# Performance work log

Hardware: AMD Instinct MI355X
Metric: run time of the kernel (lower is better)

## Reference

```python
import jax, jax.numpy as jnp
import numpy as np

B, L, D = 1, 4096, 2048
H, KV, HD = 16, 4, 128
WINDOW = 1024
ROPE_BASE = 10000.0


def _rms_norm(x, scale):
    var = jnp.mean(jnp.square(x), axis=-1, keepdims=True)
    return x * jax.lax.rsqrt(var + 1e-6) * scale


def _apply_rope(x, positions, base_frequency):
    # x: (B, L, N, HD); positions: (B, L)
    head_dim = x.shape[-1]
    half = head_dim // 2
    freq_exp = 2.0 * jnp.arange(half, dtype=jnp.float32) / head_dim
    timescale = base_frequency ** freq_exp                       # (half,)
    sinusoid = positions[..., None].astype(jnp.float32) / timescale  # (B, L, half)
    sin = jnp.sin(sinusoid)[:, :, None, :]                       # (B, L, 1, half)
    cos = jnp.cos(sinusoid)[:, :, None, :]
    x1, x2 = x[..., :half], x[..., half:]
    return jnp.concatenate([x1 * cos - x2 * sin, x2 * cos + x1 * sin], axis=-1)


def setup_inputs() -> dict:
    key = jax.random.key(0)
    ks = jax.random.split(key, 5)
    x = jax.random.normal(ks[0], (B, L, D), dtype=jnp.float32)
    positions = jnp.broadcast_to(jnp.arange(L, dtype=jnp.int32), (B, L))
    s = D ** -0.5
    Wq = jax.random.normal(ks[1], (D, H * HD), dtype=jnp.float32) * s
    Wk = jax.random.normal(ks[2], (D, KV * HD), dtype=jnp.float32) * s
    Wv = jax.random.normal(ks[3], (D, KV * HD), dtype=jnp.float32) * s
    Wo = jax.random.normal(ks[4], (H * HD, D), dtype=jnp.float32) * ((H * HD) ** -0.5)
    q_scale = jnp.ones((HD,), dtype=jnp.float32)
    k_scale = jnp.ones((HD,), dtype=jnp.float32)
    return {"x": x, "positions": positions, "Wq": Wq, "Wk": Wk, "Wv": Wv,
            "Wo": Wo, "q_scale": q_scale, "k_scale": k_scale}


def reference(x, positions, Wq, Wk, Wv, Wo, q_scale, k_scale):
    q = (x @ Wq).reshape(B, L, H, HD)
    k = (x @ Wk).reshape(B, L, KV, HD)
    v = (x @ Wv).reshape(B, L, KV, HD)

    q = _apply_rope(_rms_norm(q, q_scale), positions, ROPE_BASE)
    k = _apply_rope(_rms_norm(k, k_scale), positions, ROPE_BASE)

    rep = H // KV
    k = jnp.repeat(k, rep, axis=2)   # (B, L, H, HD)
    v = jnp.repeat(v, rep, axis=2)

    scale = HD ** -0.5
    scores = jnp.einsum('bqhd,bkhd->bhqk', q, k) * scale  # (B, H, L, L)

    idx = jnp.arange(L)
    causal = idx[:, None] >= idx[None, :]
    window = idx[None, :] >= idx[:, None] - (WINDOW - 1)
    mask = causal & window
    scores = jnp.where(mask[None, None, :, :], scores, jnp.finfo(scores.dtype).min)
    attn = jax.nn.softmax(scores, axis=-1)

    out = jnp.einsum('bhqk,bkhd->bqhd', attn, v).reshape(B, L, H * HD)
    return out @ Wo
```

## Files before the change

kernel.cpp:

```cpp
#include <hip/hip_runtime.h>
#include <cstdint>
#include <cstddef>

typedef unsigned short u16;
typedef __attribute__((ext_vector_type(4))) float  float4v;
typedef __attribute__((ext_vector_type(4))) int    int4v;
typedef __attribute__((ext_vector_type(8))) short  short8v;
typedef __attribute__((ext_vector_type(4))) short  short4v;

#define L_SEQ 4096
#define NH 16
#define NKV 4
#define WND 1024

static __device__ __forceinline__ u16 f2bf(float f) {
  union { float f; unsigned u; } v; v.f = f;
  unsigned r = (v.u + 0x7FFFu + ((v.u >> 16) & 1u)) >> 16;
  return (u16)r;
}
static __device__ __forceinline__ u16 f2bf_fast(float f) {
  union { float f; unsigned u; } v; v.f = f;
  return (u16)((v.u + 0x8000u) >> 16);
}
static __device__ __forceinline__ float bf2f(u16 b) {
  union { unsigned u; float f; } v; v.u = ((unsigned)b) << 16;
  return v.f;
}

__global__ __launch_bounds__(256) void k_cvt(const float* __restrict__ in,
                                             u16* __restrict__ out, int n4) {
  int i = blockIdx.x * 256 + threadIdx.x;
  if (i >= n4) return;
  float4v v = ((const float4v*)in)[i];
  short4v o;
  o[0] = (short)f2bf(v[0]); o[1] = (short)f2bf(v[1]);
  o[2] = (short)f2bf(v[2]); o[3] = (short)f2bf(v[3]);
  ((short4v*)out)[i] = o;
}

__global__ __launch_bounds__(256) void k_transpose64(const float* __restrict__ in,
                                                     u16* __restrict__ out,
                                                     int K, int N, int row_off) {
  __shared__ float tile[64][65];
  int n0 = blockIdx.x * 64, k0 = blockIdx.y * 64;
  int tx = threadIdx.x & 63, ty = threadIdx.x >> 6;
#pragma unroll
  for (int i = 0; i < 16; i++)
    tile[ty + i*4][tx] = in[(size_t)(k0 + ty + i*4)*N + n0 + tx];
  __syncthreads();
#pragma unroll
  for (int i = 0; i < 16; i++)
    out[(size_t)(row_off + n0 + ty + i*4)*K + k0 + tx] = f2bf(tile[tx][ty + i*4]);
}

__global__ __launch_bounds__(256) void k_vtrans(const u16* __restrict__ qkvb,
                                                u16* __restrict__ vT) {
  __shared__ u16 tile[64][66];
  int p0 = blockIdx.x * 64, d0 = blockIdx.y * 64;
  int tx = threadIdx.x & 63, ty = threadIdx.x >> 6;
#pragma unroll
  for (int i = 0; i < 16; i++)
    tile[ty + i*4][tx] = qkvb[(size_t)(p0 + ty + i*4)*3072 + 2560 + d0 + tx];
  __syncthreads();
#pragma unroll
  for (int i = 0; i < 16; i++)
    vT[(size_t)(d0 + ty + i*4)*L_SEQ + p0 + tx] = tile[tx][ty + i*4];
}

template<int BF16_OUT>
__global__ __launch_bounds__(256) void k_gemm_bt(const u16* __restrict__ A,
                                                 const u16* __restrict__ B,
                                                 void* __restrict__ Cv,
                                                 int M, int N, int K) {
  __shared__ alignas(16) u16 As[128*64];
  __shared__ alignas(16) u16 Bs[128*64];
  int tid = threadIdx.x;
  int lane = tid & 63, wave = tid >> 6;
  int lr = lane & 15, lg = lane >> 4;
  int m0 = blockIdx.y * 128, n0 = blockIdx.x * 128;
  int wm = (wave >> 1) * 64, wn = (wave & 1) * 64;

  float4v acc[4][4];
#pragma unroll
  for (int i = 0; i < 4; i++)
#pragma unroll
    for (int j = 0; j < 4; j++)
#pragma unroll
      for (int r = 0; r < 4; r++) acc[i][j][r] = 0.f;

  for (int kt = 0; kt < K; kt += 64) {
    __syncthreads();
#pragma unroll
    for (int it = 0; it < 4; it++) {
      int s = it*256 + tid;
      int row = s >> 3, j = s & 7;
      int col = ((j ^ (row & 7)) << 3);
      __builtin_amdgcn_global_load_lds(
          (const __attribute__((address_space(1))) void*)(A + (size_t)(m0 + row)*K + kt + col),
          (__attribute__((address_space(3))) void*)(&As[s * 8]), 16, 0, 0);
      __builtin_amdgcn_global_load_lds(
          (const __attribute__((address_space(1))) void*)(B + (size_t)(n0 + row)*K + kt + col),
          (__attribute__((address_space(3))) void*)(&Bs[s * 8]), 16, 0, 0);
    }
    __syncthreads();
#pragma unroll
    for (int half = 0; half < 2; half++) {
      short8v af[4], bf[4];
#pragma unroll
      for (int i = 0; i < 4; i++) {
        int row = wm + i*16 + lr;
        af[i] = *(const short8v*)(&As[row*64 + ((((half<<2)|lg) ^ (row & 7)) << 3)]);
      }
#pragma unroll
      for (int j = 0; j < 4; j++) {
        int row = wn + j*16 + lr;
        bf[j] = *(const short8v*)(&Bs[row*64 + ((((half<<2)|lg) ^ (row & 7)) << 3)]);
      }
#pragma unroll
      for (int i = 0; i < 4; i++)
#pragma unroll
        for (int j = 0; j < 4; j++)
          acc[i][j] = __builtin_amdgcn_mfma_f32_16x16x32_bf16(af[i], bf[j], acc[i][j], 0, 0, 0);
    }
  }
#pragma unroll
  for (int i = 0; i < 4; i++)
#pragma unroll
    for (int j = 0; j < 4; j++)
#pragma unroll
      for (int r = 0; r < 4; r++) {
        size_t idx = (size_t)(m0 + wm + i*16 + lg*4 + r)*N + (n0 + wn + j*16 + lr);
        if (BF16_OUT) ((u16*)Cv)[idx] = f2bf(acc[i][j][r]);
        else          ((float*)Cv)[idx] = acc[i][j][r];
      }
}

__global__ __launch_bounds__(256) void k_qknorm(const u16* __restrict__ qkvb,
    const int* __restrict__ positions, const float* __restrict__ q_scale,
    const float* __restrict__ k_scale, u16* __restrict__ qb,
    u16* __restrict__ kb) {
  int p = blockIdx.x * 4 + (threadIdx.x >> 6);
  int l = threadIdx.x & 63;
  const float LOG2_BASE = 13.287712379549449f;
  float ang = (float)positions[p] * exp2f(-(float)l * (LOG2_BASE / 64.0f));
  float sn, cs; sincosf(ang, &sn, &cs);
  float qs1 = q_scale[l], qs2 = q_scale[l + 64];
  float ks1 = k_scale[l], ks2 = k_scale[l + 64];
  const u16* base = qkvb + (size_t)p * 3072;
  const float qsc = 0.12751741505539613f;
#pragma unroll
  for (int h = 0; h < 16; h++) {
    float x1 = bf2f(base[h*128 + l]), x2 = bf2f(base[h*128 + l + 64]);
    float ss = x1*x1 + x2*x2;
#pragma unroll
    for (int m = 1; m < 64; m <<= 1) ss += __shfl_xor(ss, m);
    float rinv = rsqrtf(ss * (1.0f/128.0f) + 1e-6f);
    x1 *= rinv * qs1; x2 *= rinv * qs2;
    u16* dst = qb + ((size_t)p*NH + h)*128;
    dst[l]      = f2bf((x1*cs - x2*sn) * qsc);
    dst[l + 64] = f2bf((x2*cs + x1*sn) * qsc);
  }
#pragma unroll
  for (int g = 0; g < 4; g++) {
    float x1 = bf2f(base[2048 + g*128 + l]), x2 = bf2f(base[2048 + g*128 + l + 64]);
    float ss = x1*x1 + x2*x2;
#pragma unroll
    for (int m = 1; m < 64; m <<= 1) ss += __shfl_xor(ss, m);
    float rinv = rsqrtf(ss * (1.0f/128.0f) + 1e-6f);
    x1 *= rinv * ks1; x2 *= rinv * ks2;
    u16* dst = kb + ((size_t)p*NKV + g)*128;
    dst[l]      = f2bf(x1*cs - x2*sn);
    dst[l + 64] = f2bf(x2*cs + x1*sn);
  }
}

__global__ __launch_bounds__(256) void k_attn(const u16* __restrict__ qb,
    const u16* __restrict__ kb, const u16* __restrict__ vT,
    u16* __restrict__ ob) {
  __shared__ alignas(16) u16 Ks[64*128];
  __shared__ alignas(16) u16 Vs[128*64];
  __shared__ alignas(16) u16 Pw[4][2][16*72];
  int tid = threadIdx.x;
  int lane = tid & 63, wave = tid >> 6;
  int lr = lane & 15, lg = lane >> 4;
  int flat = blockIdx.x;
  int xcd = flat & 7, slot = flat >> 3;
  int gh = xcd >> 1;
  int q0 = ((xcd & 1) * 64 + slot) * 32;
  int h = gh * 4 + wave;

  short8v qf[2][4];
#pragma unroll
  for (int m = 0; m < 2; m++) {
    const u16* qrow = qb + ((size_t)(q0 + m*16 + lr)*NH + h)*128 + lg*8;
#pragma unroll
    for (int t = 0; t < 4; t++) qf[m][t] = *(const short8v*)(qrow + t*32);
  }

  const short one_bf = (short)0x3F80;
  const short8v ones = {one_bf,one_bf,one_bf,one_bf,one_bf,one_bf,one_bf,one_bf};

  float4v O[9][2];
#pragma unroll
  for (int dt = 0; dt < 9; dt++)
#pragma unroll
    for (int m = 0; m < 2; m++)
#pragma unroll
      for (int r = 0; r < 4; r++) O[dt][m][r] = 0.f;

  int kstart = q0 - (WND - 1); if (kstart < 0) kstart = 0; kstart &= ~63;
  for (int kt = kstart; kt < q0 + 32; kt += 64) {
    __syncthreads();
#pragma unroll
    for (int it = 0; it < 4; it++) {
      int s = it*256 + tid;
      { int row = s >> 4, j = s & 15, col = (j ^ (row & 15)) << 3;
        __builtin_amdgcn_global_load_lds(
            (const __attribute__((address_space(1))) void*)(kb + (size_t)(kt + row)*512 + gh*128 + col),
            (__attribute__((address_space(3))) void*)(&Ks[s * 8]), 16, 0, 0); }
      { int row = s >> 3, j = s & 7, col = (j ^ (row & 7)) << 3;
        __builtin_amdgcn_global_load_lds(
            (const __attribute__((address_space(1))) void*)(vT + (size_t)(gh*128 + row)*L_SEQ + kt + col),
            (__attribute__((address_space(3))) void*)(&Vs[s * 8]), 16, 0, 0); }
    }
    __syncthreads();

    float4v S[2][4];
#pragma unroll
    for (int m = 0; m < 2; m++)
#pragma unroll
      for (int t2 = 0; t2 < 4; t2++)
#pragma unroll
        for (int r = 0; r < 4; r++) S[m][t2][r] = 0.f;
#pragma unroll
    for (int t2 = 0; t2 < 4; t2++) {
      int row = t2*16 + lr;
#pragma unroll
      for (int t = 0; t < 4; t++) {
        short8v kf = *(const short8v*)(&Ks[row*128 + (((t*4 + lg) ^ (row & 15)) << 3)]);
        S[0][t2] = __builtin_amdgcn_mfma_f32_16x16x32_bf16(qf[0][t], kf, S[0][t2], 0, 0, 0);
        S[1][t2] = __builtin_amdgcn_mfma_f32_16x16x32_bf16(qf[1][t], kf, S[1][t2], 0, 0, 0);
      }
    }

    bool need_mask = (kt + 64 > q0) || (kt < q0 - (WND - 32));
    if (need_mask) {
#pragma unroll
      for (int m = 0; m < 2; m++)
#pragma unroll
        for (int r = 0; r < 4; r++) {
          int pos = q0 + m*16 + lg*4 + r;
#pragma unroll
          for (int t2 = 0; t2 < 4; t2++) {
            int key = kt + t2*16 + lr;
            float p = (key > pos || key < pos - (WND - 1)) ? 0.f : exp2f(S[m][t2][r]);
            Pw[wave][m][(lg*4 + r)*72 + t2*16 + lr] = f2bf_fast(p);
          }
        }
    } else {
#pragma unroll
      for (int m = 0; m < 2; m++)
#pragma unroll
        for (int r = 0; r < 4; r++)
#pragma unroll
          for (int t2 = 0; t2 < 4; t2++)
            Pw[wave][m][(lg*4 + r)*72 + t2*16 + lr] = f2bf_fast(exp2f(S[m][t2][r]));
    }

    short8v pf[2][2];
#pragma unroll
    for (int m = 0; m < 2; m++)
#pragma unroll
      for (int sub = 0; sub < 2; sub++)
        pf[m][sub] = *(const short8v*)(&Pw[wave][m][lr*72 + sub*32 + lg*8]);

#pragma unroll
    for (int sub = 0; sub < 2; sub++)
#pragma unroll
      for (int dt = 0; dt < 8; dt++) {
        int row = dt*16 + lr;
        short8v vf = *(const short8v*)(&Vs[row*64 + (((sub*4 + lg) ^ (row & 7)) << 3)]);
        O[dt][0] = __builtin_amdgcn_mfma_f32_16x16x32_bf16(pf[0][sub], vf, O[dt][0], 0, 0, 0);
        O[dt][1] = __builtin_amdgcn_mfma_f32_16x16x32_bf16(pf[1][sub], vf, O[dt][1], 0, 0, 0);
      }
#pragma unroll
    for (int m = 0; m < 2; m++) {
      O[8][m] = __builtin_amdgcn_mfma_f32_16x16x32_bf16(pf[m][0], ones, O[8][m], 0, 0, 0);
      O[8][m] = __builtin_amdgcn_mfma_f32_16x16x32_bf16(pf[m][1], ones, O[8][m], 0, 0, 0);
    }
  }

#pragma unroll
  for (int m = 0; m < 2; m++)
#pragma unroll
    for (int r = 0; r < 4; r++) {
      float inv = 1.0f / O[8][m][r];
#pragma unroll
      for (int dt = 0; dt < 8; dt++)
        ob[((size_t)(q0 + m*16 + lg*4 + r)*NH + h)*128 + dt*16 + lr] =
            f2bf(O[dt][m][r] * inv);
    }
}

extern "C" void kernel_launch(void* const* d_in, const int* in_sizes, int n_in,
                              void* d_out, int out_size, void* d_ws, size_t ws_size,
                              hipStream_t stream) {
  (void)in_sizes; (void)n_in; (void)out_size; (void)ws_size;
  const float* x        = (const float*)d_in[0];
  const int*   positions= (const int*)d_in[1];
  const float* Wq       = (const float*)d_in[2];
  const float* Wk       = (const float*)d_in[3];
  const float* Wv       = (const float*)d_in[4];
  const float* Wo       = (const float*)d_in[5];
  const float* q_scale  = (const float*)d_in[6];
  const float* k_scale  = (const float*)d_in[7];
  float* out = (float*)d_out;

  char* ws = (char*)d_ws;
  u16* xb   = (u16*)ws; ws += (size_t)4096*2048*2;
  u16* Wt   = (u16*)ws; ws += (size_t)3072*2048*2;
  u16* Wot  = (u16*)ws; ws += (size_t)2048*2048*2;
  u16* qkvb = (u16*)ws; ws += (size_t)4096*3072*2;
  u16* qb   = (u16*)ws; ws += (size_t)4096*2048*2;
  u16* kb   = (u16*)ws; ws += (size_t)4096*512*2;
  u16* vT   = (u16*)ws; ws += (size_t)4096*512*2;
  u16* ob   = qkvb;

  k_cvt<<<8192, 256, 0, stream>>>(x, xb, 2097152);
  k_transpose64<<<dim3(32,32), 256, 0, stream>>>(Wq, Wt, 2048, 2048, 0);
  k_transpose64<<<dim3(8,32),  256, 0, stream>>>(Wk, Wt, 2048, 512, 2048);
  k_transpose64<<<dim3(8,32),  256, 0, stream>>>(Wv, Wt, 2048, 512, 2560);
  k_transpose64<<<dim3(32,32), 256, 0, stream>>>(Wo, Wot, 2048, 2048, 0);
  k_gemm_bt<1><<<dim3(24,32), 256, 0, stream>>>(xb, Wt, qkvb, 4096, 3072, 2048);
  k_qknorm<<<1024, 256, 0, stream>>>(qkvb, positions, q_scale, k_scale, qb, kb);
  k_vtrans<<<dim3(64,8), 256, 0, stream>>>(qkvb, vT);
  k_attn<<<512, 256, 0, stream>>>(qb, kb, vT, ob);
  k_gemm_bt<0><<<dim3(16,32), 256, 0, stream>>>(ob, Wot, out, 4096, 2048, 2048);
}
```

Measured before the change: 296.7 us.

## Replace GEMM with 256x256 double-buffered 8-wave pipelined kernel

Replaces the 128x128 single-buffered GEMM with a 256x256 tile kernel using 8 waves, double-buffered LDS, and staged global-to-LDS loads interleaved with MFMA phases. It also remaps workgroups into XCD-aware chunks and raises MFMA priority with setprio. The goal is to hide load latency behind compute and raise data reuse per tile. In exchange, the grid shrinks to 192 and 128 workgroups, which may underfill the 256 CUs, and LDS use rises to 128KB per block.

```diff
diff --git a/kernel.cpp b/kernel.cpp
--- a/kernel.cpp
+++ b/kernel.cpp
@@ -67,71 +67,169 @@
     vT[(size_t)(d0 + ty + i*4)*L_SEQ + p0 + tx] = tile[tx][ty + i*4];
 }
 
-template<int BF16_OUT>
-__global__ __launch_bounds__(256) void k_gemm_bt(const u16* __restrict__ A,
-                                                 const u16* __restrict__ B,
-                                                 void* __restrict__ Cv,
-                                                 int M, int N, int K) {
-  __shared__ alignas(16) u16 As[128*64];
-  __shared__ alignas(16) u16 Bs[128*64];
+template<int KDIM>
+static __device__ __forceinline__ void stage_half(const u16* __restrict__ g,
+                                                  u16* lds, int tid) {
+#pragma unroll
+  for (int it = 0; it < 2; ++it) {
+    int s = it * 512 + tid;
+    int row = s >> 3, slot = s & 7;
+    __builtin_amdgcn_global_load_lds(
+        (const __attribute__((address_space(1))) void*)(g + (size_t)row * KDIM + ((slot ^ (row & 7)) << 3)),
+        (__attribute__((address_space(3))) void*)(lds + s * 8), 16, 0, 0);
+  }
+}
+
+template<int BF16_OUT, int KDIM>
+__global__ __launch_bounds__(512, 2) void k_gemm8(const u16* __restrict__ A,
+                                                  const u16* __restrict__ B,
+                                                  void* __restrict__ Cv,
+                                                  int N) {
+  constexpr int NT = KDIM >> 6;
+  __shared__ alignas(16) u16 As[2][256 * 64];
+  __shared__ alignas(16) u16 Bs[2][256 * 64];
   int tid = threadIdx.x;
   int lane = tid & 63, wave = tid >> 6;
   int lr = lane & 15, lg = lane >> 4;
-  int m0 = blockIdx.y * 128, n0 = blockIdx.x * 128;
-  int wm = (wave >> 1) * 64, wn = (wave & 1) * 64;
-
-  float4v acc[4][4];
-#pragma unroll
-  for (int i = 0; i < 4; i++)
+  int wm = (wave >> 2) * 128, wn = (wave & 3) * 64;
+
+  int nwg = gridDim.x * gridDim.y;
+  int orig = blockIdx.y * gridDim.x + blockIdx.x;
+  int cpx = nwg >> 3;
+  int wg = (orig & 7) * cpx + (orig >> 3);
+  int tn = wg % gridDim.x, tm = wg / gridDim.x;
+  int m0 = tm * 256, n0 = tn * 256;
+
+  const u16* Ag = A + (size_t)m0 * KDIM;
+  const u16* Bg = B + (size_t)n0 * KDIM;
+
+  float4v acc[8][4];
+#pragma unroll
+  for (int i = 0; i < 8; i++)
 #pragma unroll
     for (int j = 0; j < 4; j++)
 #pragma unroll
       for (int r = 0; r < 4; r++) acc[i][j][r] = 0.f;
 
-  for (int kt = 0; kt < K; kt += 64) {
-    __syncthreads();
-#pragma unroll
-    for (int it = 0; it < 4; it++) {
-      int s = it*256 + tid;
-      int row = s >> 3, j = s & 7;
-      int col = ((j ^ (row & 7)) << 3);
-      __builtin_amdgcn_global_load_lds(
-          (const __attribute__((address_space(1))) void*)(A + (size_t)(m0 + row)*K + kt + col),
-          (__attribute__((address_space(3))) void*)(&As[s * 8]), 16, 0, 0);
-      __builtin_amdgcn_global_load_lds(
-          (const __attribute__((address_space(1))) void*)(B + (size_t)(n0 + row)*K + kt + col),
-          (__attribute__((address_space(3))) void*)(&Bs[s * 8]), 16, 0, 0);
-    }
-    __syncthreads();
-#pragma unroll
-    for (int half = 0; half < 2; half++) {
-      short8v af[4], bf[4];
-#pragma unroll
-      for (int i = 0; i < 4; i++) {
-        int row = wm + i*16 + lr;
-        af[i] = *(const short8v*)(&As[row*64 + ((((half<<2)|lg) ^ (row & 7)) << 3)]);
-      }
-#pragma unroll
-      for (int j = 0; j < 4; j++) {
-        int row = wn + j*16 + lr;
-        bf[j] = *(const short8v*)(&Bs[row*64 + ((((half<<2)|lg) ^ (row & 7)) << 3)]);
-      }
-#pragma unroll
-      for (int i = 0; i < 4; i++)
-#pragma unroll
-        for (int j = 0; j < 4; j++)
-          acc[i][j] = __builtin_amdgcn_mfma_f32_16x16x32_bf16(af[i], bf[j], acc[i][j], 0, 0, 0);
-    }
-  }
-#pragma unroll
-  for (int i = 0; i < 4; i++)
-#pragma unroll
-    for (int j = 0; j < 4; j++)
-#pragma unroll
-      for (int r = 0; r < 4; r++) {
-        size_t idx = (size_t)(m0 + wm + i*16 + lg*4 + r)*N + (n0 + wn + j*16 + lr);
-        if (BF16_OUT) ((u16*)Cv)[idx] = f2bf(acc[i][j][r]);
-        else          ((float*)Cv)[idx] = acc[i][j][r];
+  stage_half<KDIM>(Ag,                          &As[0][0],    tid);
+  stage_half<KDIM>(Ag + (size_t)128 * KDIM,     &As[0][8192], tid);
+  stage_half<KDIM>(Bg,                          &Bs[0][0],    tid);
+  stage_half<KDIM>(Bg + (size_t)128 * KDIM,     &Bs[0][8192], tid);
+  stage_half<KDIM>(Bg + 64,                     &Bs[1][0],    tid);
+  stage_half<KDIM>(Bg + (size_t)128 * KDIM + 64,&Bs[1][8192], tid);
+  asm volatile("s_waitcnt vmcnt(4)" ::: "memory");
+  __builtin_amdgcn_s_barrier();
+
+#pragma unroll 2
+  for (int t = 0; t < NT; ++t) {
+    int cur = t & 1;
+    const u16* Asc = &As[cur][0];
+    const u16* Bsc = &Bs[cur][0];
+    u16* Asn = &As[cur ^ 1][0];
+    u16* Bsp = &Bs[cur][0];
+    short8v a[4][2], b0[2][2], b1[2][2];
+
+#pragma unroll
+    for (int i = 0; i < 4; ++i) {
+      int r = wm + i * 16 + lr;
+#pragma unroll
+      for (int ks = 0; ks < 2; ++ks)
+        a[i][ks] = *(const short8v*)(Asc + r * 64 + ((((ks << 2) | lg) ^ (r & 7)) << 3));
+    }
+#pragma unroll
+    for (int j = 0; j < 2; ++j) {
+      int r = wn + j * 16 + lr;
+#pragma unroll
+      for (int ks = 0; ks < 2; ++ks)
+        b0[j][ks] = *(const short8v*)(Bsc + r * 64 + ((((ks << 2) | lg) ^ (r & 7)) << 3));
+    }
+    if (t + 1 < NT)
+      stage_half<KDIM>(Ag + (size_t)(t + 1) * 64, Asn, tid);
+    __builtin_amdgcn_s_barrier();
+    asm volatile("s_waitcnt lgkmcnt(0)" ::: "memory");
+    __builtin_amdgcn_sched_barrier(0);
+    __builtin_amdgcn_s_setprio(1);
+#pragma unroll
+    for (int i = 0; i < 4; ++i)
+#pragma unroll
+      for (int j = 0; j < 2; ++j)
+#pragma unroll
+        for (int ks = 0; ks < 2; ++ks)
+          acc[i][j] = __builtin_amdgcn_mfma_f32_16x16x32_bf16(a[i][ks], b0[j][ks], acc[i][j], 0, 0, 0);
+    __builtin_amdgcn_s_setprio(0);
+    __builtin_amdgcn_s_barrier();
+
+#pragma unroll
+    for (int j = 0; j < 2; ++j) {
+      int r = wn + (2 + j) * 16 + lr;
+#pragma unroll
+      for (int ks = 0; ks < 2; ++ks)
+        b1[j][ks] = *(const short8v*)(Bsc + r * 64 + ((((ks << 2) | lg) ^ (r & 7)) << 3));
+    }
+    if (t + 1 < NT)
+      stage_half<KDIM>(Ag + (size_t)128 * KDIM + (size_t)(t + 1) * 64, Asn + 8192, tid);
+    __builtin_amdgcn_s_barrier();
+    asm volatile("s_waitcnt lgkmcnt(0)" ::: "memory");
+    __builtin_amdgcn_sched_barrier(0);
+    __builtin_amdgcn_s_setprio(1);
+#pragma unroll
+    for (int i = 0; i < 4; ++i)
+#pragma unroll
+      for (int j = 0; j < 2; ++j)
+#pragma unroll
+        for (int ks = 0; ks < 2; ++ks)
+          acc[i][2 + j] = __builtin_amdgcn_mfma_f32_16x16x32_bf16(a[i][ks], b1[j][ks], acc[i][2 + j], 0, 0, 0);
+    __builtin_amdgcn_s_setprio(0);
+    __builtin_amdgcn_s_barrier();
+
+#pragma unroll
+    for (int i = 0; i < 4; ++i) {
+      int r = wm + 64 + i * 16 + lr;
+#pragma unroll
+      for (int ks = 0; ks < 2; ++ks)
+        a[i][ks] = *(const short8v*)(Asc + r * 64 + ((((ks << 2) | lg) ^ (r & 7)) << 3));
+    }
+    if (t + 2 < NT)
+      stage_half<KDIM>(Bg + (size_t)(t + 2) * 64, Bsp, tid);
+    __builtin_amdgcn_s_barrier();
+    asm volatile("s_waitcnt lgkmcnt(0)" ::: "memory");
+    __builtin_amdgcn_sched_barrier(0);
+    __builtin_amdgcn_s_setprio(1);
+#pragma unroll
+    for (int i = 0; i < 4; ++i)
+#pragma unroll
+      for (int j = 0; j < 2; ++j)
+#pragma unroll
+        for (int ks = 0; ks < 2; ++ks)
+          acc[4 + i][2 + j] = __builtin_amdgcn_mfma_f32_16x16x32_bf16(a[i][ks], b1[j][ks], acc[4 + i][2 + j], 0, 0, 0);
+    __builtin_amdgcn_s_setprio(0);
+    __builtin_amdgcn_s_barrier();
+
+    if (t + 2 < NT)
+      stage_half<KDIM>(Bg + (size_t)128 * KDIM + (size_t)(t + 2) * 64, Bsp + 8192, tid);
+    asm volatile("s_waitcnt vmcnt(4)" ::: "memory");
+    __builtin_amdgcn_s_barrier();
+    __builtin_amdgcn_s_setprio(1);
+#pragma unroll
+    for (int i = 0; i < 4; ++i)
+#pragma unroll
+      for (int j = 0; j < 2; ++j)
+#pragma unroll
+        for (int ks = 0; ks < 2; ++ks)
+          acc[4 + i][j] = __builtin_amdgcn_mfma_f32_16x16x32_bf16(a[i][ks], b0[j][ks], acc[4 + i][j], 0, 0, 0);
+    __builtin_amdgcn_s_setprio(0);
+    __builtin_amdgcn_s_barrier();
+  }
+
+#pragma unroll
+  for (int mi = 0; mi < 8; ++mi)
+#pragma unroll
+    for (int ni = 0; ni < 4; ++ni)
+#pragma unroll
+      for (int r = 0; r < 4; ++r) {
+        size_t idx = (size_t)(m0 + wm + mi * 16 + lg * 4 + r) * N + (n0 + wn + ni * 16 + lr);
+        if (BF16_OUT) ((u16*)Cv)[idx] = f2bf(acc[mi][ni][r]);
+        else          ((float*)Cv)[idx] = acc[mi][ni][r];
       }
 }
 
@@ -331,9 +429,9 @@
   k_transpose64<<<dim3(8,32),  256, 0, stream>>>(Wk, Wt, 2048, 512, 2048);
   k_transpose64<<<dim3(8,32),  256, 0, stream>>>(Wv, Wt, 2048, 512, 2560);
   k_transpose64<<<dim3(32,32), 256, 0, stream>>>(Wo, Wot, 2048, 2048, 0);
-  k_gemm_bt<1><<<dim3(24,32), 256, 0, stream>>>(xb, Wt, qkvb, 4096, 3072, 2048);
+  k_gemm8<1, 2048><<<dim3(12,16), 512, 0, stream>>>(xb, Wt, qkvb, 3072);
   k_qknorm<<<1024, 256, 0, stream>>>(qkvb, positions, q_scale, k_scale, qb, kb);
   k_vtrans<<<dim3(64,8), 256, 0, stream>>>(qkvb, vT);
   k_attn<<<512, 256, 0, stream>>>(qb, kb, vT, ob);
-  k_gemm_bt<0><<<dim3(16,32), 256, 0, stream>>>(ob, Wot, out, 4096, 2048, 2048);
-}
+  k_gemm8<0, 2048><<<dim3(8,16), 512, 0, stream>>>(ob, Wot, out, 2048);
+}
```

After: 314.3 us. 5.9% more time.

## Double-buffer K/V tiles in attention kernel and raise MFMA wave priority

Applied to the files above, without the earlier changes.

The attention kernel now keeps two LDS buffers for the K and V tiles. It prefetches the next key tile with global_load_lds while the current tile is computed, using explicit vmcnt waits and raw barriers in place of the two __syncthreads per iteration. s_setprio is raised around the MFMA sections to favour matrix work over other waves. This doubles K/V LDS use, which can reduce occupancy, and relies on the manual waitcnt counts being correct.

```diff
diff --git a/kernel.cpp b/kernel.cpp
--- a/kernel.cpp
+++ b/kernel.cpp
@@ -177,8 +177,8 @@
 __global__ __launch_bounds__(256) void k_attn(const u16* __restrict__ qb,
     const u16* __restrict__ kb, const u16* __restrict__ vT,
     u16* __restrict__ ob) {
-  __shared__ alignas(16) u16 Ks[64*128];
-  __shared__ alignas(16) u16 Vs[128*64];
+  __shared__ alignas(16) u16 Ks[2][64*128];
+  __shared__ alignas(16) u16 Vs[2][128*64];
   __shared__ alignas(16) u16 Pw[4][2][16*72];
   int tid = threadIdx.x;
   int lane = tid & 63, wave = tid >> 6;
@@ -209,21 +209,46 @@
       for (int r = 0; r < 4; r++) O[dt][m][r] = 0.f;
 
   int kstart = q0 - (WND - 1); if (kstart < 0) kstart = 0; kstart &= ~63;
-  for (int kt = kstart; kt < q0 + 32; kt += 64) {
-    __syncthreads();
-#pragma unroll
-    for (int it = 0; it < 4; it++) {
-      int s = it*256 + tid;
-      { int row = s >> 4, j = s & 15, col = (j ^ (row & 15)) << 3;
-        __builtin_amdgcn_global_load_lds(
-            (const __attribute__((address_space(1))) void*)(kb + (size_t)(kt + row)*512 + gh*128 + col),
-            (__attribute__((address_space(3))) void*)(&Ks[s * 8]), 16, 0, 0); }
-      { int row = s >> 3, j = s & 7, col = (j ^ (row & 7)) << 3;
-        __builtin_amdgcn_global_load_lds(
-            (const __attribute__((address_space(1))) void*)(vT + (size_t)(gh*128 + row)*L_SEQ + kt + col),
-            (__attribute__((address_space(3))) void*)(&Vs[s * 8]), 16, 0, 0); }
-    }
-    __syncthreads();
+  int kend = q0 + 32;
+
+#pragma unroll
+  for (int it = 0; it < 4; it++) {
+    int s = it*256 + tid;
+    { int row = s >> 4, j = s & 15, col = (j ^ (row & 15)) << 3;
+      __builtin_amdgcn_global_load_lds(
+          (const __attribute__((address_space(1))) void*)(kb + (size_t)(kstart + row)*512 + gh*128 + col),
+          (__attribute__((address_space(3))) void*)(&Ks[0][s * 8]), 16, 0, 0); }
+    { int row = s >> 3, j = s & 7, col = (j ^ (row & 7)) << 3;
+      __builtin_amdgcn_global_load_lds(
+          (const __attribute__((address_space(1))) void*)(vT + (size_t)(gh*128 + row)*L_SEQ + kstart + col),
+          (__attribute__((address_space(3))) void*)(&Vs[0][s * 8]), 16, 0, 0); }
+  }
+
+  int par = 0;
+  for (int kt = kstart; kt < kend; kt += 64, par ^= 1) {
+    if (kt + 64 < kend) {
+      int kn = kt + 64, pn = par ^ 1;
+#pragma unroll
+      for (int it = 0; it < 4; it++) {
+        int s = it*256 + tid;
+        { int row = s >> 4, j = s & 15, col = (j ^ (row & 15)) << 3;
+          __builtin_amdgcn_global_load_lds(
+              (const __attribute__((address_space(1))) void*)(kb + (size_t)(kn + row)*512 + gh*128 + col),
+              (__attribute__((address_space(3))) void*)(&Ks[pn][s * 8]), 16, 0, 0); }
+        { int row = s >> 3, j = s & 7, col = (j ^ (row & 7)) << 3;
+          __builtin_amdgcn_global_load_lds(
+              (const __attribute__((address_space(1))) void*)(vT + (size_t)(gh*128 + row)*L_SEQ + kn + col),
+              (__attribute__((address_space(3))) void*)(&Vs[pn][s * 8]), 16, 0, 0); }
+      }
+      asm volatile("s_waitcnt vmcnt(8)" ::: "memory");
+    } else {
+      asm volatile("s_waitcnt vmcnt(0)" ::: "memory");
+    }
+    __builtin_amdgcn_s_barrier();
+    asm volatile("" ::: "memory");
+
+    const u16* ksP = &Ks[par][0];
+    const u16* vsP = &Vs[par][0];
 
     float4v S[2][4];
 #pragma unroll
@@ -232,16 +257,18 @@
       for (int t2 = 0; t2 < 4; t2++)
 #pragma unroll
         for (int r = 0; r < 4; r++) S[m][t2][r] = 0.f;
+    __builtin_amdgcn_s_setprio(1);
 #pragma unroll
     for (int t2 = 0; t2 < 4; t2++) {
       int row = t2*16 + lr;
 #pragma unroll
       for (int t = 0; t < 4; t++) {
-        short8v kf = *(const short8v*)(&Ks[row*128 + (((t*4 + lg) ^ (row & 15)) << 3)]);
+        short8v kf = *(const short8v*)(&ksP[row*128 + (((t*4 + lg) ^ (row & 15)) << 3)]);
         S[0][t2] = __builtin_amdgcn_mfma_f32_16x16x32_bf16(qf[0][t], kf, S[0][t2], 0, 0, 0);
         S[1][t2] = __builtin_amdgcn_mfma_f32_16x16x32_bf16(qf[1][t], kf, S[1][t2], 0, 0, 0);
       }
     }
+    __builtin_amdgcn_s_setprio(0);
 
     bool need_mask = (kt + 64 > q0) || (kt < q0 - (WND - 32));
     if (need_mask) {
@@ -274,12 +301,13 @@
       for (int sub = 0; sub < 2; sub++)
         pf[m][sub] = *(const short8v*)(&Pw[wave][m][lr*72 + sub*32 + lg*8]);
 
+    __builtin_amdgcn_s_setprio(1);
 #pragma unroll
     for (int sub = 0; sub < 2; sub++)
 #pragma unroll
       for (int dt = 0; dt < 8; dt++) {
         int row = dt*16 + lr;
-        short8v vf = *(const short8v*)(&Vs[row*64 + (((sub*4 + lg) ^ (row & 7)) << 3)]);
+        short8v vf = *(const short8v*)(&vsP[row*64 + (((sub*4 + lg) ^ (row & 7)) << 3)]);
         O[dt][0] = __builtin_amdgcn_mfma_f32_16x16x32_bf16(pf[0][sub], vf, O[dt][0], 0, 0, 0);
         O[dt][1] = __builtin_amdgcn_mfma_f32_16x16x32_bf16(pf[1][sub], vf, O[dt][1], 0, 0, 0);
       }
@@ -288,6 +316,10 @@
       O[8][m] = __builtin_amdgcn_mfma_f32_16x16x32_bf16(pf[m][0], ones, O[8][m], 0, 0, 0);
       O[8][m] = __builtin_amdgcn_mfma_f32_16x16x32_bf16(pf[m][1], ones, O[8][m], 0, 0, 0);
     }
+    __builtin_amdgcn_s_setprio(0);
+
+    asm volatile("" ::: "memory");
+    __builtin_amdgcn_s_barrier();
   }
 
 #pragma unroll
```

After: 322.7 us. +8.8%, slower.
